# Optimization experiments

Hardware: AMD Instinct MI355X
Metric: run time of the kernel (lower is better)

## Reference

```python
import jax, jax.numpy as jnp
import numpy as np

B_SZ, L_SEQ, H_CH, N_ST = 8, 4096, 256, 64


def setup_inputs() -> dict:
    key = jax.random.key(0)
    ks = jax.random.split(key, 12)
    rn = lambda k, s, sc=1.0: jax.random.normal(k, s, jnp.float32) * sc
    inp = {
        'x': rn(ks[0], (B_SZ, L_SEQ, H_CH)),
        # stable DPLR spectrum: Re(Lambda) < 0, HiPPO-like imaginary ladder
        'Lambda_re': -(jnp.abs(rn(ks[1], (N_ST,))) + 0.1),
        'Lambda_im': jnp.pi * jnp.arange(N_ST, dtype=jnp.float32),
        'P_re': rn(ks[2], (N_ST,), N_ST ** -0.5),
        'P_im': rn(ks[3], (N_ST,), N_ST ** -0.5),
        'Q_re': rn(ks[4], (N_ST,), N_ST ** -0.5),
        'Q_im': rn(ks[5], (N_ST,), N_ST ** -0.5),
        'B_re': rn(ks[6], (N_ST,), N_ST ** -0.5),
        'B_im': rn(ks[7], (N_ST,), N_ST ** -0.5),
        'C_re': rn(ks[8], (H_CH, N_ST), N_ST ** -0.5),
        'C_im': rn(ks[9], (H_CH, N_ST), N_ST ** -0.5),
        'step': jnp.ones((1,), jnp.float32) * 1e-3,
        'D': jnp.zeros((1,), jnp.float32),
        'W_fc': rn(ks[10], (H_CH, H_CH), H_CH ** -0.5),
        'b_fc': jnp.zeros((H_CH,), jnp.float32),
        'ln_g': jnp.ones((H_CH,), jnp.float32),
        'ln_b': jnp.zeros((H_CH,), jnp.float32),
    }
    return inp


def _dplr_kernel(Lambda_re, Lambda_im, P_re, P_im, Q_re, Q_im, B_re, B_im, C_re, C_im, step, L):
    # S4 DPLR generating function evaluated at the L roots of unity (torch_get_K_derta).
    Lam = (Lambda_re + 1j * Lambda_im).astype(jnp.complex64)  # (N,)
    Pc = (P_re + 1j * P_im).astype(jnp.complex64)
    Qc = (Q_re + 1j * Q_im).astype(jnp.complex64)
    Bc = (B_re + 1j * B_im).astype(jnp.complex64)
    Cc = (C_re + 1j * C_im).astype(jnp.complex64)  # (H, N)
    k = jnp.arange(L, dtype=jnp.float32)
    Omega = jnp.exp((-2j * jnp.pi) * (k / L)).astype(jnp.complex64)  # (L,)
    c = 2.0 / (1.0 + Omega)
    g = (2.0 / step[0]) * (1.0 - Omega) / (1.0 + Omega)  # bilinear transform points, (L,)
    inv = 1.0 / (g[:, None] - Lam[None, :])  # Cauchy matrix, (L, N)
    k00 = jnp.einsum('hn,ln->hl', Cc * Bc[None, :], inv)  # (H, L)
    k01 = jnp.einsum('hn,ln->hl', Cc * Pc[None, :], inv)
    k10 = jnp.einsum('n,ln->l', Qc * Bc, inv)  # (L,)
    k11 = jnp.einsum('n,ln->l', Qc * Pc, inv)
    atRoots = c[None, :] * (k00 - k01 * (k10 / (1.0 + k11))[None, :])  # Woodbury correction
    K = jnp.fft.ifft(atRoots, axis=-1).real  # (H, L)
    return K.astype(jnp.float32)


def reference(x, Lambda_re, Lambda_im, P_re, P_im, Q_re, Q_im, B_re, B_im, C_re, C_im, step, D, W_fc, b_fc, ln_g, ln_b):
    Bsz, L, H = x.shape
    step = jnp.maximum(step, 1e-6)
    K = _dplr_kernel(Lambda_re, Lambda_im, P_re, P_im, Q_re, Q_im, B_re, B_im, C_re, C_im, step, L)  # (H, L)
    # causal FFT convolution per channel (torch_convolution with fft=True)
    n = 2 * L
    Kf = jnp.fft.rfft(K, n=n, axis=-1)           # (H, F)
    uf = jnp.fft.rfft(x, n=n, axis=1)            # (B, F, H)
    h1 = jnp.fft.irfft(uf * Kf.T[None], n=n, axis=1)[:, :L, :]
    y1 = jax.nn.gelu(h1 + D * x, approximate=False)  # mult_activation='gelu'
    y2 = jax.nn.gelu(y1 @ W_fc.T + b_fc, approximate=False)  # fc + final_act
    y2 = y2 + x  # skip
    mu = jnp.mean(y2, axis=-1, keepdims=True)
    var = jnp.var(y2, axis=-1, keepdims=True)
    y = (y2 - mu) / jnp.sqrt(var + 1e-5) * ln_g + ln_b  # LayerNorm; dropout p=0
    h_ratio = jnp.max(jnp.abs(y), axis=1) / (jnp.max(jnp.abs(x), axis=1) + 1e-6)  # (B, H)
    return y, h_ratio
```

## Files before the change

### kernel.cpp

```cpp
#include <hip/hip_runtime.h>
#include <math.h>

typedef float2 cf;
typedef __attribute__((ext_vector_type(8))) short bf16x8;
typedef __attribute__((ext_vector_type(4))) float f32x4;

__device__ __forceinline__ cf cmk(float x, float y){ cf r; r.x=x; r.y=y; return r; }
__device__ __forceinline__ cf cml(cf a, cf b){ return cmk(a.x*b.x - a.y*b.y, a.x*b.y + a.y*b.x); }
__device__ __forceinline__ cf cad(cf a, cf b){ return cmk(a.x+b.x, a.y+b.y); }
__device__ __forceinline__ cf csb(cf a, cf b){ return cmk(a.x-b.x, a.y-b.y); }
__device__ __forceinline__ cf cjg(cf a){ return cmk(a.x, -a.y); }
__device__ __forceinline__ cf crcp(cf d){ float r = 1.0f/(d.x*d.x + d.y*d.y); return cmk(d.x*r, -d.y*r); }
__device__ __forceinline__ cf cdv(cf n, cf d){ return cml(n, crcp(d)); }
__device__ __forceinline__ float geluf(float z){ return 0.5f*z*(1.0f + erff(z*0.70710678118654752f)); }

__device__ __forceinline__ cf twid(float f, float sign){
  float h = f * 0.5f;
  float s = __builtin_amdgcn_sinf(h);
  float c0 = __builtin_amdgcn_cosf(h);
  return cmk(c0, sign * s);
}

__device__ __forceinline__ void bfsplit(float v, ushort* h, ushort* l){
  unsigned u = __float_as_uint(v);
  unsigned hr = (u + 0x7FFFu + ((u >> 16) & 1u)) & 0xFFFF0000u;
  *h = (ushort)(hr >> 16);
  float lv = v - __uint_as_float(hr);
  unsigned u2 = __float_as_uint(lv);
  *l = (ushort)((u2 + 0x7FFFu + ((u2 >> 16) & 1u)) >> 16);
}

__device__ __forceinline__ void dif4q(cf& q0, cf& q1, cf& q2, cf& q3, cf w1, float sign){
  cf w2 = cml(w1, w1);
  cf a1 = cad(q0, q2);
  cf c1 = cml(csb(q0, q2), w1);
  cf b1 = cad(q1, q3);
  cf d1 = cml(csb(q1, q3), cmk(-sign*w1.y, sign*w1.x));
  q0 = cad(a1, b1);
  q1 = cml(csb(a1, b1), w2);
  q2 = cad(c1, d1);
  q3 = cml(csb(c1, d1), w2);
}
__device__ __forceinline__ void dit4q(cf& q0, cf& q1, cf& q2, cf& q3, cf w1, float sign){
  cf w2 = cml(w1, w1);
  cf t1 = cml(q1, w2);
  cf a1 = cad(q0, t1), b1 = csb(q0, t1);
  cf t2 = cml(q3, w2);
  cf c1 = cad(q2, t2), d1 = csb(q2, t2);
  cf v1 = cml(c1, w1);
  cf v2 = cml(d1, cmk(-sign*w1.y, sign*w1.x));
  q0 = cad(a1, v1);
  q2 = csb(a1, v1);
  q1 = cad(b1, v2);
  q3 = csb(b1, v2);
}
__device__ __forceinline__ void dif4q0(cf& q0, cf& q1, cf& q2, cf& q3, float sign){
  cf a1 = cad(q0, q2), c1 = csb(q0, q2);
  cf b1 = cad(q1, q3), d0 = csb(q1, q3);
  cf d1 = cmk(-sign*d0.y, sign*d0.x);
  q0 = cad(a1, b1); q1 = csb(a1, b1);
  q2 = cad(c1, d1); q3 = csb(c1, d1);
}
__device__ __forceinline__ void dit4q0(cf& q0, cf& q1, cf& q2, cf& q3, float sign){
  cf a1 = cad(q0, q1), b1 = csb(q0, q1);
  cf c1 = cad(q2, q3), d0 = csb(q2, q3);
  cf v2 = cmk(-sign*d0.y, sign*d0.x);
  q0 = cad(a1, c1); q2 = csb(a1, c1);
  q1 = cad(b1, v2); q3 = csb(b1, v2);
}

__device__ __forceinline__ int brev12(int x){ return (int)(__brev((unsigned)x) >> 20); }
__device__ __forceinline__ int brev13(int x){ return (int)(__brev((unsigned)x) >> 19); }
__device__ __forceinline__ int pidx(int n){ return n + 4*(n>>8); }

template<int N, int SSTART, int TP>
__device__ void fft_dif_r4(cf* __restrict__ a, float sign){
  #pragma unroll
  for (int s = SSTART; s >= 1; s >>= 2){
    __syncthreads();
    #pragma unroll
    for (int g = 0; g < (N >> 2) / TP; g++){
      int w = (int)threadIdx.x + g * TP;
      int j = w & (s - 1);
      int base = ((w & ~(s - 1)) << 2) | j;
      cf A0 = a[base], B0 = a[base + s], C0 = a[base + 2*s], D0 = a[base + 3*s];
      cf w1 = twid((float)j / (float)(2 * s), sign);
      cf w2 = cml(w1, w1);
      cf a1 = cad(A0, C0);
      cf c1 = cml(csb(A0, C0), w1);
      cf b1 = cad(B0, D0);
      cf d1 = cml(csb(B0, D0), cmk(-sign * w1.y, sign * w1.x));
      a[base]         = cad(a1, b1);
      a[base + s]     = cml(csb(a1, b1), w2);
      a[base + 2*s]   = cad(c1, d1);
      a[base + 3*s]   = cml(csb(c1, d1), w2);
    }
  }
  if constexpr ((__builtin_ctz(N) & 1) == 1){
    __syncthreads();
    #pragma unroll
    for (int g = 0; g < (N >> 1) / TP; g++){
      int w = (int)threadIdx.x + g * TP;
      int i = w << 1;
      cf u = a[i], v = a[i + 1];
      a[i] = cad(u, v);
      a[i + 1] = csb(u, v);
    }
  }
  __syncthreads();
}

template<int N, int TP>
__device__ void fft_dit_r4(cf* __restrict__ a, float sign){
  if constexpr ((__builtin_ctz(N) & 1) == 1){
    __syncthreads();
    #pragma unroll
    for (int g = 0; g < (N >> 1) / TP; g++){
      int w = (int)threadIdx.x + g * TP;
      int i = w << 1;
      cf u = a[i], v = a[i + 1];
      a[i] = cad(u, v);
      a[i + 1] = csb(u, v);
    }
  }
  constexpr int S0 = ((__builtin_ctz(N) & 1) == 1) ? 2 : 1;
  #pragma unroll
  for (int s = S0; s <= (N >> 2); s <<= 2){
    __syncthreads();
    #pragma unroll
    for (int g = 0; g < (N >> 2) / TP; g++){
      int w = (int)threadIdx.x + g * TP;
      int j = w & (s - 1);
      int base = ((w & ~(s - 1)) << 2) | j;
      cf A0 = a[base], B0 = a[base + s], C0 = a[base + 2*s], D0 = a[base + 3*s];
      cf w1 = twid((float)j / (float)(2 * s), sign);
      cf w2 = cml(w1, w1);
      cf t1 = cml(B0, w2);
      cf a1 = cad(A0, t1), b1 = csb(A0, t1);
      cf t2 = cml(D0, w2);
      cf c1 = cad(C0, t2), d1 = csb(C0, t2);
      cf v1 = cml(c1, w1);
      cf v2 = cml(d1, cmk(-sign * w1.y, sign * w1.x));
      a[base]         = cad(a1, v1);
      a[base + 2*s]   = csb(a1, v1);
      a[base + s]     = cad(b1, v2);
      a[base + 3*s]   = csb(b1, v2);
    }
  }
  __syncthreads();
}

template<int TP>
__device__ void dif8192_pad_stage(cf* __restrict__ a, float sign){
  __syncthreads();
  #pragma unroll
  for (int g = 0; g < 2048 / TP; g++){
    int w = (int)threadIdx.x + g * TP;
    cf A0 = a[w], B0 = a[w + 2048];
    cf w1 = twid((float)w * (1.0f / 4096.0f), sign);
    cf w2 = cml(w1, w1);
    cf c1 = cml(A0, w1);
    cf d1 = cml(B0, cmk(-sign * w1.y, sign * w1.x));
    a[w]        = cad(A0, B0);
    a[w + 2048] = cml(csb(A0, B0), w2);
    a[w + 4096] = cad(c1, d1);
    a[w + 6144] = cml(csb(c1, d1), w2);
  }
}

__global__ void k_init(unsigned* xmax, unsigned* ymax){
  int i = blockIdx.x * 256 + threadIdx.x;
  if (i < 2048){ xmax[i] = 0u; ymax[i] = 0u; }
}

__global__ __launch_bounds__(256) void k_transpose_x(const float* __restrict__ x,
                                                     float* __restrict__ xT,
                                                     unsigned* __restrict__ xmax){
  __shared__ float tile[64][65];
  __shared__ float red[64][4];
  int b = blockIdx.z;
  int t0 = blockIdx.x * 64;
  int h0 = blockIdx.y * 64;
  int hc = threadIdx.x & 63, tg = threadIdx.x >> 6;
  float pmax = 0.0f;
  #pragma unroll
  for (int q = 0; q < 16; q++){
    int tr = tg + q * 4;
    float v = x[((size_t)(b * 4096 + t0 + tr)) * 256 + h0 + hc];
    tile[tr][hc] = v;
    pmax = fmaxf(pmax, fabsf(v));
  }
  red[hc][tg] = pmax;
  __syncthreads();
  if (threadIdx.x < 64){
    float m = fmaxf(fmaxf(red[threadIdx.x][0], red[threadIdx.x][1]),
                    fmaxf(red[threadIdx.x][2], red[threadIdx.x][3]));
    atomicMax(&xmax[b * 256 + h0 + threadIdx.x], __float_as_uint(m));
  }
  #pragma unroll
  for (int q = 0; q < 16; q++){
    int hr = tg + q * 4;
    xT[((size_t)(b * 256 + h0 + hr)) * 4096 + t0 + hc] = tile[hc][hr];
  }
}

__global__ void k_wsplit(const float* __restrict__ W, ushort* __restrict__ Wh, ushort* __restrict__ Wl){
  int i = blockIdx.x * 256 + threadIdx.x;
  ushort h, l;
  bfsplit(W[i], &h, &l);
  Wh[i] = h; Wl[i] = l;
}

__global__ __launch_bounds__(256) void k_cauchy(
    const float* __restrict__ Lr, const float* __restrict__ Li,
    const float* __restrict__ Pr, const float* __restrict__ Pi,
    const float* __restrict__ Qr, const float* __restrict__ Qi,
    const float* __restrict__ Br, const float* __restrict__ Bi,
    const float* __restrict__ Cr, const float* __restrict__ Ci,
    const float* __restrict__ stepp, cf* __restrict__ A)
{
  __shared__ cf sLam[64], sB[64], sP[64], sQB[64], sQP[64];
  __shared__ cf sInv[64][16];
  __shared__ cf sWood[16], sC[16], sG[16];
  int tid = threadIdx.x;
  int l0 = blockIdx.x * 16;
  float stepv = fmaxf(stepp[0], 1e-6f);
  if (tid < 64){
    cf lam = cmk(Lr[tid], Li[tid]);
    cf b = cmk(Br[tid], Bi[tid]);
    cf p = cmk(Pr[tid], Pi[tid]);
    cf q = cmk(Qr[tid], Qi[tid]);
    sLam[tid] = lam; sB[tid] = b; sP[tid] = p;
    sQB[tid] = cml(q, b);
    sQP[tid] = cml(q, p);
  }
  __syncthreads();
  if (tid < 16){
    int l = l0 + tid;
    float ang = -6.2831855f * ((float)l * (1.0f / 4096.0f));
    cf Om = cmk(cosf(ang), sinf(ang));
    cf den = cmk(1.0f + Om.x, Om.y);
    cf num = cmk(1.0f - Om.x, -Om.y);
    cf rden = crcp(den);
    sC[tid] = cml(cmk(2.0f, 0.0f), rden);
    cf g = cml(num, rden);
    float sc = 2.0f / stepv;
    sG[tid] = cmk(g.x * sc, g.y * sc);
  }
  __syncthreads();
  for (int it = tid; it < 1024; it += 256){
    int n = it >> 4, ll = it & 15;
    sInv[n][ll] = crcp(csb(sG[ll], sLam[n]));
  }
  __syncthreads();
  if (tid < 16){
    cf k10 = cmk(0,0), k11 = cmk(0,0);
    for (int n = 0; n < 64; n++){
      k10 = cad(k10, cml(sQB[n], sInv[n][tid]));
      k11 = cad(k11, cml(sQP[n], sInv[n][tid]));
    }
    sWood[tid] = cdv(k10, cmk(1.0f + k11.x, k11.y));
  }
  __syncthreads();
  int h = tid;
  cf a0[16], a1[16];
  #pragma unroll
  for (int ll = 0; ll < 16; ll++){ a0[ll] = cmk(0,0); a1[ll] = cmk(0,0); }
  for (int n = 0; n < 64; n++){
    cf cc = cmk(Cr[h * 64 + n], Ci[h * 64 + n]);
    cf cb = cml(cc, sB[n]);
    cf cp = cml(cc, sP[n]);
    #pragma unroll
    for (int ll = 0; ll < 16; ll++){
      cf iv = sInv[n][ll];
      a0[ll] = cad(a0[ll], cml(cb, iv));
      a1[ll] = cad(a1[ll], cml(cp, iv));
    }
  }
  cf* dst = A + (size_t)h * 4096 + l0;
  #pragma unroll
  for (int ll = 0; ll < 16; ll++){
    dst[ll] = cml(sC[ll], csb(a0[ll], cml(a1[ll], sWood[ll])));
  }
}

__global__ __launch_bounds__(512) void k_kf(const cf* __restrict__ A, float4* __restrict__ Sab){
  extern __shared__ cf c[];
  int hp = blockIdx.x, tid = threadIdx.x;
  const cf* a1p = A + (size_t)(2 * hp) * 4096;
  const cf* a2p = a1p + 4096;
  for (int l = tid; l < 4096; l += 512){
    int r = brev12(l);
    cf u = a1p[l], w = a2p[l];
    c[r] = cmk(u.x - w.y, u.y + w.x);
  }
  fft_dit_r4<4096, 512>(c, 1.0f);
  float k1[8], k2[8];
  #pragma unroll
  for (int q = 0; q < 8; q++){
    cf w = c[tid + q * 512];
    k1[q] = w.x * (1.0f / 4096.0f);
    k2[q] = w.y * (1.0f / 4096.0f);
  }
  __syncthreads();
  #pragma unroll
  for (int q = 0; q < 8; q++) c[tid + q * 512] = cmk(k1[q], k2[q]);
  dif8192_pad_stage<512>(c, -1.0f);
  fft_dif_r4<8192, 512, 512>(c, -1.0f);
  float4* rec = Sab + (size_t)hp * 4097;
  const float sc = 0.5f * 0.5f * (1.0f / 8192.0f);
  #pragma unroll
  for (int q8 = 0; q8 < 8; q8++){
    int t = tid + 512 * q8;
    int p = t << 1;
    int k = brev13(p);
    int qq = brev13((8192 - k) & 8191);
    cf Zp = c[p], Zq = c[qq];
    float K1x = (Zp.x + Zq.x), K1y = (Zp.y - Zq.y);
    float dx  = (Zp.x - Zq.x), dy  = (Zp.y + Zq.y);
    float K2x = dy, K2y = -dx;
    rec[t] = make_float4((K1x + K2x) * sc, (K1y + K2y) * sc,
                         (K1x - K2x) * sc, (K1y - K2y) * sc);
  }
  if (tid == 0){
    cf Z1 = c[1];
    float K1x = 2.0f * Z1.x, K2x = 2.0f * Z1.y;
    rec[4096] = make_float4((K1x + K2x) * sc, 0.0f, (K1x - K2x) * sc, 0.0f);
  }
}

__global__ __launch_bounds__(256) void k_conv(const float* __restrict__ xT,
                                              const float4* __restrict__ Sab,
                                              const float* __restrict__ Dp,
                                              ushort* __restrict__ y1h,
                                              ushort* __restrict__ y1l){
  __shared__ __align__(16) cf c[8320];
  int blk = blockIdx.x;
  int b = blk >> 7, hp = blk & 127;
  int t = threadIdx.x;
  int lo4 = t & 15, hiT = t >> 4;
  int base0 = lo4 + ((hiT << 1) << 8);
  int base1 = lo4 + ((((hiT << 1) | 1)) << 8);
  int cb0 = pidx((t << 1) << 4);
  int cb1 = pidx(((t << 1) | 1) << 4);
  const float* xs1 = xT + ((size_t)(b * 256 + 2 * hp)) * 4096;
  const float* xs2 = xs1 + 4096;
  cf v[32];
  #pragma unroll
  for (int r = 0; r < 16; r++){
    int n = t + 256 * r;
    v[r] = cmk(xs1[n], xs2[n]);
  }
  #pragma unroll
  for (int r = 0; r < 16; r++)
    v[r + 16] = cml(v[r], twid((float)(t + 256 * r) * (1.0f / 4096.0f), -1.0f));
  #pragma unroll
  for (int r0 = 0; r0 < 4; r0++){
    cf w1 = twid((float)(t + 256 * r0) * (1.0f / 2048.0f), -1.0f);
    dif4q(v[r0], v[r0 + 4], v[r0 + 8], v[r0 + 12], w1, -1.0f);
    dif4q(v[16 + r0], v[16 + r0 + 4], v[16 + r0 + 8], v[16 + r0 + 12], w1, -1.0f);
  }
  {
    cf w1 = twid((float)t * (1.0f / 512.0f), -1.0f);
    #pragma unroll
    for (int g = 0; g < 32; g += 4)
      dif4q(v[g], v[g + 1], v[g + 2], v[g + 3], w1, -1.0f);
  }
  #pragma unroll
  for (int r = 0; r < 32; r++) c[pidx(t + 256 * r)] = v[r];
  __syncthreads();
  #pragma unroll
  for (int u = 0; u < 16; u++){
    v[u]      = c[pidx(base0 + (u << 4))];
    v[16 + u] = c[pidx(base1 + (u << 4))];
  }
  #pragma unroll
  for (int u0 = 0; u0 < 4; u0++){
    cf w1 = twid((float)(lo4 + (u0 << 4)) * (1.0f / 128.0f), -1.0f);
    dif4q(v[u0], v[u0 + 4], v[u0 + 8], v[u0 + 12], w1, -1.0f);
    dif4q(v[16 + u0], v[16 + u0 + 4], v[16 + u0 + 8], v[16 + u0 + 12], w1, -1.0f);
  }
  {
    cf w1 = twid((float)lo4 * (1.0f / 32.0f), -1.0f);
    #pragma unroll
    for (int g = 0; g < 32; g += 4)
      dif4q(v[g], v[g + 1], v[g + 2], v[g + 3], w1, -1.0f);
  }
  #pragma unroll
  for (int u = 0; u < 16; u++){
    c[pidx(base0 + (u << 4))] = v[u];
    c[pidx(base1 + (u << 4))] = v[16 + u];
  }
  __syncthreads();
  #pragma unroll
  for (int k = 0; k < 8; k++){
    float4 q0 = *(const float4*)&c[cb0 + 2 * k];
    float4 q1 = *(const float4*)&c[cb1 + 2 * k];
    v[2 * k]      = cmk(q0.x, q0.y); v[2 * k + 1]      = cmk(q0.z, q0.w);
    v[16 + 2 * k] = cmk(q1.x, q1.y); v[16 + 2 * k + 1] = cmk(q1.z, q1.w);
  }
  #pragma unroll
  for (int u0 = 0; u0 < 4; u0++){
    cf w1 = twid((float)u0 * 0.125f, -1.0f);
    dif4q(v[u0], v[u0 + 4], v[u0 + 8], v[u0 + 12], w1, -1.0f);
    dif4q(v[16 + u0], v[16 + u0 + 4], v[16 + u0 + 8], v[16 + u0 + 12], w1, -1.0f);
  }
  #pragma unroll
  for (int g = 0; g < 32; g += 4) dif4q0(v[g], v[g + 1], v[g + 2], v[g + 3], -1.0f);
  #pragma unroll
  for (int k = 0; k < 8; k++){
    *(float4*)&c[cb0 + 2 * k] = make_float4(v[2*k].x, v[2*k].y, v[2*k+1].x, v[2*k+1].y);
    *(float4*)&c[cb1 + 2 * k] = make_float4(v[16+2*k].x, v[16+2*k].y, v[16+2*k+1].x, v[16+2*k+1].y);
  }
  __syncthreads();
  {
    const float4* rec = Sab + (size_t)hp * 4097;
    #pragma unroll
    for (int q8 = 0; q8 < 16; q8++){
      int th = t + 256 * q8;
      int p = th << 1;
      int k = brev13(p);
      int qq = brev13((8192 - k) & 8191);
      int pi = pidx(p), qi = pidx(qq);
      cf Zp = c[pi], Zq = c[qi];
      float4 r0 = rec[th];
      cf Sap = cmk(r0.x, r0.y), Sbp = cmk(r0.z, r0.w);
      c[pi] = cad(cml(Zp, Sap), cml(cjg(Zq), Sbp));
      c[qi] = cad(cml(Zq, cjg(Sap)), cml(cjg(Zp), cjg(Sbp)));
    }
    if (t == 0){
      float4 e = rec[4096];
      cf Z1 = c[pidx(1)];
      c[pidx(1)] = cad(cml(Z1, cmk(e.x, e.y)), cml(cjg(Z1), cmk(e.z, e.w)));
    }
  }
  __syncthreads();
  #pragma unroll
  for (int k = 0; k < 8; k++){
    float4 q0 = *(const float4*)&c[cb0 + 2 * k];
    float4 q1 = *(const float4*)&c[cb1 + 2 * k];
    v[2 * k]      = cmk(q0.x, q0.y); v[2 * k + 1]      = cmk(q0.z, q0.w);
    v[16 + 2 * k] = cmk(q1.x, q1.y); v[16 + 2 * k + 1] = cmk(q1.z, q1.w);
  }
  #pragma unroll
  for (int g = 0; g < 32; g += 4) dit4q0(v[g], v[g + 1], v[g + 2], v[g + 3], 1.0f);
  #pragma unroll
  for (int u0 = 0; u0 < 4; u0++){
    cf w1 = twid((float)u0 * 0.125f, 1.0f);
    dit4q(v[u0], v[u0 + 4], v[u0 + 8], v[u0 + 12], w1, 1.0f);
    dit4q(v[16 + u0], v[16 + u0 + 4], v[16 + u0 + 8], v[16 + u0 + 12], w1, 1.0f);
  }
  #pragma unroll
  for (int k = 0; k < 8; k++){
    *(float4*)&c[cb0 + 2 * k] = make_float4(v[2*k].x, v[2*k].y, v[2*k+1].x, v[2*k+1].y);
    *(float4*)&c[cb1 + 2 * k] = make_float4(v[16+2*k].x, v[16+2*k].y, v[16+2*k+1].x, v[16+2*k+1].y);
  }
  __syncthreads();
  #pragma unroll
  for (int u = 0; u < 16; u++){
    v[u]      = c[pidx(base0 + (u << 4))];
    v[16 + u] = c[pidx(base1 + (u << 4))];
  }
  {
    cf w1 = twid((float)lo4 * (1.0f / 32.0f), 1.0f);
    #pragma unroll
    for (int g = 0; g < 32; g += 4)
      dit4q(v[g], v[g + 1], v[g + 2], v[g + 3], w1, 1.0f);
  }
  #pragma unroll
  for (int u0 = 0; u0 < 4; u0++){
    cf w1 = twid((float)(lo4 + (u0 << 4)) * (1.0f / 128.0f), 1.0f);
    dit4q(v[u0], v[u0 + 4], v[u0 + 8], v[u0 + 12], w1, 1.0f);
    dit4q(v[16 + u0], v[16 + u0 + 4], v[16 + u0 + 8], v[16 + u0 + 12], w1, 1.0f);
  }
  #pragma unroll
  for (int u = 0; u < 16; u++){
    c[pidx(base0 + (u << 4))] = v[u];
    c[pidx(base1 + (u << 4))] = v[16 + u];
  }
  __syncthreads();
  #pragma unroll
  for (int r = 0; r < 32; r++) v[r] = c[pidx(t + 256 * r)];
  {
    cf w1 = twid((float)t * (1.0f / 512.0f), 1.0f);
    #pragma unroll
    for (int g = 0; g < 32; g += 4)
      dit4q(v[g], v[g + 1], v[g + 2], v[g + 3], w1, 1.0f);
  }
  #pragma unroll
  for (int r0 = 0; r0 < 4; r0++){
    cf w1 = twid((float)(t + 256 * r0) * (1.0f / 2048.0f), 1.0f);
    dit4q(v[r0], v[r0 + 4], v[r0 + 8], v[r0 + 12], w1, 1.0f);
    dit4q(v[16 + r0], v[16 + r0 + 4], v[16 + r0 + 8], v[16 + r0 + 12], w1, 1.0f);
  }
  float Dv = Dp[0];
  size_t base = ((size_t)(b * 256 + 2 * hp)) * 4096;
  #pragma unroll
  for (int r = 0; r < 16; r++){
    int n = t + 256 * r;
    cf w = cad(v[r], cml(v[r + 16], twid((float)n * (1.0f / 4096.0f), 1.0f)));
    float z1 = geluf(fmaf(Dv, xs1[n], w.x));
    float z2 = geluf(fmaf(Dv, xs2[n], w.y));
    ushort h0, l0, h1u, l1;
    bfsplit(z1, &h0, &l0);
    bfsplit(z2, &h1u, &l1);
    y1h[base + n] = h0;         y1l[base + n] = l0;
    y1h[base + 4096 + n] = h1u; y1l[base + 4096 + n] = l1;
  }
}

__global__ __launch_bounds__(256, 3) void k_gemm_ln(
    const ushort* __restrict__ y1h, const ushort* __restrict__ y1l,
    const ushort* __restrict__ Wh, const ushort* __restrict__ Wl,
    const float* __restrict__ bfc, const float* __restrict__ x,
    const float* __restrict__ lng, const float* __restrict__ lnb,
    float* __restrict__ yout, unsigned* __restrict__ ymax)
{
  __shared__ ushort sY[2][64 * 40];
  __shared__ float red1[64][4], red2[64][4];
  int tid = threadIdx.x;
  int l = tid & 63;
  int w = tid >> 6;
  int blk = blockIdx.x;
  int b = blk >> 6;
  int t0 = (blk & 63) * 64;
  int g = l >> 4, cc = l & 15;

  f32x4 acc[4][4];
  #pragma unroll
  for (int m = 0; m < 4; m++)
    #pragma unroll
    for (int n = 0; n < 4; n++)
      acc[m][n] = (f32x4){0.0f, 0.0f, 0.0f, 0.0f};

  int kk = tid >> 3, ts = (tid & 7) * 8;

  #pragma unroll 1
  for (int kc = 0; kc < 256; kc += 32){
    __syncthreads();
    {
      size_t gb = ((size_t)(b * 256 + kc + kk)) * 4096 + t0 + ts;
      float4 vh = *(const float4*)(y1h + gb);
      float4 vl = *(const float4*)(y1l + gb);
      const ushort* ph = (const ushort*)&vh;
      const ushort* pl = (const ushort*)&vl;
      int kblk = kk >> 3, kin = kk & 7;
      #pragma unroll
      for (int e = 0; e < 8; e++){
        int t = ts + e;
        int idx = t * 40 + ((kblk ^ ((t >> 3) & 3)) << 3) + kin;
        sY[0][idx] = ph[e];
        sY[1][idx] = pl[e];
      }
    }
    __syncthreads();
    bf16x8 afh[4], afl[4];
    #pragma unroll
    for (int m = 0; m < 4; m++){
      int t = m * 16 + cc;
      int idx = t * 40 + ((g ^ ((t >> 3) & 3)) << 3);
      afh[m] = *(bf16x8*)&sY[0][idx];
      afl[m] = *(bf16x8*)&sY[1][idx];
    }
    #pragma unroll
    for (int n = 0; n < 4; n++){
      size_t wj = (size_t)(w * 64 + n * 16 + cc) * 256 + kc + g * 8;
      bf16x8 bh = *(const bf16x8*)(Wh + wj);
      bf16x8 bl = *(const bf16x8*)(Wl + wj);
      #pragma unroll
      for (int m = 0; m < 4; m++){
        acc[m][n] = __builtin_amdgcn_mfma_f32_16x16x32_bf16(afh[m], bh, acc[m][n], 0, 0, 0);
        acc[m][n] = __builtin_amdgcn_mfma_f32_16x16x32_bf16(afh[m], bl, acc[m][n], 0, 0, 0);
        acc[m][n] = __builtin_amdgcn_mfma_f32_16x16x32_bf16(afl[m], bh, acc[m][n], 0, 0, 0);
      }
    }
  }

  float bj[4], gj[4], lj[4];
  #pragma unroll
  for (int n = 0; n < 4; n++){
    int j = w * 64 + n * 16 + cc;
    bj[n] = bfc[j]; gj[n] = lng[j]; lj[n] = lnb[j];
  }
  #pragma unroll
  for (int m = 0; m < 4; m++){
    #pragma unroll
    for (int r = 0; r < 4; r++){
      int tl = m * 16 + g * 4 + r;
      size_t rowb = ((size_t)(b * 4096 + t0 + tl)) * 256;
      float ss = 0.0f, sq = 0.0f;
      #pragma unroll
      for (int n = 0; n < 4; n++){
        float z = geluf(acc[m][n][r] + bj[n]) + x[rowb + w * 64 + n * 16 + cc];
        acc[m][n][r] = z;
        ss += z; sq = fmaf(z, z, sq);
      }
      #pragma unroll
      for (int msk = 1; msk < 16; msk <<= 1){
        ss += __shfl_xor(ss, msk);
        sq += __shfl_xor(sq, msk);
      }
      if (cc == 0){ red1[tl][w] = ss; red2[tl][w] = sq; }
    }
  }
  __syncthreads();
  float jm[4] = {0.0f, 0.0f, 0.0f, 0.0f};
  #pragma unroll
  for (int m = 0; m < 4; m++){
    #pragma unroll
    for (int r = 0; r < 4; r++){
      int tl = m * 16 + g * 4 + r;
      float ts1 = red1[tl][0] + red1[tl][1] + red1[tl][2] + red1[tl][3];
      float ts2 = red2[tl][0] + red2[tl][1] + red2[tl][2] + red2[tl][3];
      float mu = ts1 * (1.0f / 256.0f);
      float var = ts2 * (1.0f / 256.0f) - mu * mu;
      float rstd = rsqrtf(var + 1e-5f);
      size_t rowb = ((size_t)(b * 4096 + t0 + tl)) * 256;
      #pragma unroll
      for (int n = 0; n < 4; n++){
        float yv = (acc[m][n][r] - mu) * rstd * gj[n] + lj[n];
        yout[rowb + w * 64 + n * 16 + cc] = yv;
        jm[n] = fmaxf(jm[n], fabsf(yv));
      }
    }
  }
  #pragma unroll
  for (int n = 0; n < 4; n++){
    jm[n] = fmaxf(jm[n], __shfl_xor(jm[n], 16));
    jm[n] = fmaxf(jm[n], __shfl_xor(jm[n], 32));
  }
  if (g == 0){
    #pragma unroll
    for (int n = 0; n < 4; n++)
      atomicMax(&ymax[b * 256 + w * 64 + n * 16 + cc], __float_as_uint(jm[n]));
  }
}

__global__ void k_ratio(const unsigned* __restrict__ ymax, const unsigned* __restrict__ xmax,
                        float* __restrict__ out){
  int i = blockIdx.x * 256 + threadIdx.x;
  if (i < 2048){
    float ym = __uint_as_float(ymax[i]);
    float xm = __uint_as_float(xmax[i]);
    out[8388608 + i] = ym / (xm + 1e-6f);
  }
}

extern "C" void kernel_launch(void* const* d_in, const int* in_sizes, int n_in,
                              void* d_out, int out_size, void* d_ws, size_t ws_size,
                              hipStream_t stream)
{
  const float* x    = (const float*)d_in[0];
  const float* Lr   = (const float*)d_in[1];
  const float* Li   = (const float*)d_in[2];
  const float* Pr   = (const float*)d_in[3];
  const float* Pi   = (const float*)d_in[4];
  const float* Qr   = (const float*)d_in[5];
  const float* Qi   = (const float*)d_in[6];
  const float* Br   = (const float*)d_in[7];
  const float* Bi   = (const float*)d_in[8];
  const float* Cr   = (const float*)d_in[9];
  const float* Ci   = (const float*)d_in[10];
  const float* stp  = (const float*)d_in[11];
  const float* Dp   = (const float*)d_in[12];
  const float* Wfc  = (const float*)d_in[13];
  const float* bfc  = (const float*)d_in[14];
  const float* lng  = (const float*)d_in[15];
  const float* lnb  = (const float*)d_in[16];

  char* ws = (char*)d_ws;
  float*    xT   = (float*)(ws);
  float4*   Sab  = (float4*)(ws + ((size_t)32 << 20));
  cf*       A    = (cf*)(ws + ((size_t)41 << 20));
  ushort*   y1h  = (ushort*)(ws + ((size_t)41 << 20));
  ushort*   y1l  = (ushort*)(ws + ((size_t)57 << 20));
  ushort*   Wh   = (ushort*)(ws + ((size_t)73 << 20));
  ushort*   Wl   = (ushort*)(ws + ((size_t)73 << 20) + (128u << 10));
  unsigned* xmax = (unsigned*)(ws + ((size_t)73 << 20) + (256u << 10));
  unsigned* ymax = xmax + 2048;

  k_init<<<8, 256, 0, stream>>>(xmax, ymax);
  dim3 gt(64, 4, 8);
  k_transpose_x<<<gt, 256, 0, stream>>>(x, xT, xmax);
  k_wsplit<<<256, 256, 0, stream>>>(Wfc, Wh, Wl);
  k_cauchy<<<256, 256, 0, stream>>>(Lr, Li, Pr, Pi, Qr, Qi, Br, Bi, Cr, Ci, stp, A);
  k_kf<<<128, 512, 65536, stream>>>(A, Sab);
  k_conv<<<1024, 256, 0, stream>>>(xT, Sab, Dp, y1h, y1l);
  k_gemm_ln<<<512, 256, 0, stream>>>(y1h, y1l, Wh, Wl, bfc, x, lng, lnb, (float*)d_out, ymax);
  k_ratio<<<8, 256, 0, stream>>>(ymax, xmax, (float*)d_out);
}
```

Measured before the change: 215.3 us.

## Use packed f32 complex ops, fold init into wsplit, widen k_kf blocks

Complex add, sub and mul helpers are rewritten with inline v_pk_add_f32, v_pk_mul_f32 and v_pk_fma_f32 asm, so each complex op uses packed two-lane instructions. The separate k_init launch is removed and the max-buffer zeroing moves into k_wsplit, which now runs before the transpose. k_kf goes from 512 to 1024 threads per block so each of its 128 blocks has more parallelism. Inline asm can block compiler scheduling and fusion, and the larger block may raise register pressure.

```diff
diff --git a/kernel.cpp b/kernel.cpp
--- a/kernel.cpp
+++ b/kernel.cpp
@@ -2,13 +2,33 @@
 #include <math.h>
 
 typedef float2 cf;
+typedef float vf2 __attribute__((ext_vector_type(2)));
 typedef __attribute__((ext_vector_type(8))) short bf16x8;
 typedef __attribute__((ext_vector_type(4))) float f32x4;
 
 __device__ __forceinline__ cf cmk(float x, float y){ cf r; r.x=x; r.y=y; return r; }
-__device__ __forceinline__ cf cml(cf a, cf b){ return cmk(a.x*b.x - a.y*b.y, a.x*b.y + a.y*b.x); }
-__device__ __forceinline__ cf cad(cf a, cf b){ return cmk(a.x+b.x, a.y+b.y); }
-__device__ __forceinline__ cf csb(cf a, cf b){ return cmk(a.x-b.x, a.y-b.y); }
+
+__device__ __forceinline__ cf cad(cf a, cf b){
+  vf2 av, bv, rv;
+  av.x = a.x; av.y = a.y; bv.x = b.x; bv.y = b.y;
+  asm("v_pk_add_f32 %0, %1, %2" : "=v"(rv) : "v"(av), "v"(bv));
+  return cmk(rv.x, rv.y);
+}
+__device__ __forceinline__ cf csb(cf a, cf b){
+  vf2 av, bv, rv;
+  av.x = a.x; av.y = a.y; bv.x = b.x; bv.y = b.y;
+  asm("v_pk_add_f32 %0, %1, %2 neg_lo:[0,1] neg_hi:[0,1]" : "=v"(rv) : "v"(av), "v"(bv));
+  return cmk(rv.x, rv.y);
+}
+__device__ __forceinline__ cf cml(cf a, cf b){
+  vf2 av, bv, rv;
+  av.x = a.x; av.y = a.y; bv.x = b.x; bv.y = b.y;
+  asm("v_pk_mul_f32 %0, %1, %2 op_sel:[0,0] op_sel_hi:[0,1]\n\t"
+      "v_pk_fma_f32 %0, %1, %2, %0 op_sel:[1,1,0] op_sel_hi:[1,0,1] neg_lo:[1,0,0]"
+      : "=&v"(rv) : "v"(av), "v"(bv));
+  return cmk(rv.x, rv.y);
+}
+
 __device__ __forceinline__ cf cjg(cf a){ return cmk(a.x, -a.y); }
 __device__ __forceinline__ cf crcp(cf d){ float r = 1.0f/(d.x*d.x + d.y*d.y); return cmk(d.x*r, -d.y*r); }
 __device__ __forceinline__ cf cdv(cf n, cf d){ return cml(n, crcp(d)); }
@@ -168,11 +188,6 @@
   }
 }
 
-__global__ void k_init(unsigned* xmax, unsigned* ymax){
-  int i = blockIdx.x * 256 + threadIdx.x;
-  if (i < 2048){ xmax[i] = 0u; ymax[i] = 0u; }
-}
-
 __global__ __launch_bounds__(256) void k_transpose_x(const float* __restrict__ x,
                                                      float* __restrict__ xT,
                                                      unsigned* __restrict__ xmax){
@@ -204,8 +219,10 @@
   }
 }
 
-__global__ void k_wsplit(const float* __restrict__ W, ushort* __restrict__ Wh, ushort* __restrict__ Wl){
+__global__ void k_wsplit(const float* __restrict__ W, ushort* __restrict__ Wh, ushort* __restrict__ Wl,
+                         unsigned* __restrict__ xmax, unsigned* __restrict__ ymax){
   int i = blockIdx.x * 256 + threadIdx.x;
+  if (i < 2048){ xmax[i] = 0u; ymax[i] = 0u; }
   ushort h, l;
   bfsplit(W[i], &h, &l);
   Wh[i] = h; Wl[i] = l;
@@ -284,34 +301,34 @@
   }
 }
 
-__global__ __launch_bounds__(512) void k_kf(const cf* __restrict__ A, float4* __restrict__ Sab){
+__global__ __launch_bounds__(1024) void k_kf(const cf* __restrict__ A, float4* __restrict__ Sab){
   extern __shared__ cf c[];
   int hp = blockIdx.x, tid = threadIdx.x;
   const cf* a1p = A + (size_t)(2 * hp) * 4096;
   const cf* a2p = a1p + 4096;
-  for (int l = tid; l < 4096; l += 512){
+  for (int l = tid; l < 4096; l += 1024){
     int r = brev12(l);
     cf u = a1p[l], w = a2p[l];
     c[r] = cmk(u.x - w.y, u.y + w.x);
   }
-  fft_dit_r4<4096, 512>(c, 1.0f);
-  float k1[8], k2[8];
-  #pragma unroll
-  for (int q = 0; q < 8; q++){
-    cf w = c[tid + q * 512];
+  fft_dit_r4<4096, 1024>(c, 1.0f);
+  float k1[4], k2[4];
+  #pragma unroll
+  for (int q = 0; q < 4; q++){
+    cf w = c[tid + q * 1024];
     k1[q] = w.x * (1.0f / 4096.0f);
     k2[q] = w.y * (1.0f / 4096.0f);
   }
   __syncthreads();
   #pragma unroll
-  for (int q = 0; q < 8; q++) c[tid + q * 512] = cmk(k1[q], k2[q]);
-  dif8192_pad_stage<512>(c, -1.0f);
-  fft_dif_r4<8192, 512, 512>(c, -1.0f);
+  for (int q = 0; q < 4; q++) c[tid + q * 1024] = cmk(k1[q], k2[q]);
+  dif8192_pad_stage<1024>(c, -1.0f);
+  fft_dif_r4<8192, 512, 1024>(c, -1.0f);
   float4* rec = Sab + (size_t)hp * 4097;
   const float sc = 0.5f * 0.5f * (1.0f / 8192.0f);
   #pragma unroll
-  for (int q8 = 0; q8 < 8; q8++){
-    int t = tid + 512 * q8;
+  for (int q8 = 0; q8 < 4; q8++){
+    int t = tid + 1024 * q8;
     int p = t << 1;
     int k = brev13(p);
     int qq = brev13((8192 - k) & 8191);
@@ -679,12 +696,11 @@
   unsigned* xmax = (unsigned*)(ws + ((size_t)73 << 20) + (256u << 10));
   unsigned* ymax = xmax + 2048;
 
-  k_init<<<8, 256, 0, stream>>>(xmax, ymax);
+  k_wsplit<<<256, 256, 0, stream>>>(Wfc, Wh, Wl, xmax, ymax);
   dim3 gt(64, 4, 8);
   k_transpose_x<<<gt, 256, 0, stream>>>(x, xT, xmax);
-  k_wsplit<<<256, 256, 0, stream>>>(Wfc, Wh, Wl);
   k_cauchy<<<256, 256, 0, stream>>>(Lr, Li, Pr, Pi, Qr, Qi, Br, Bi, Cr, Ci, stp, A);
-  k_kf<<<128, 512, 65536, stream>>>(A, Sab);
+  k_kf<<<128, 1024, 65536, stream>>>(A, Sab);
   k_conv<<<1024, 256, 0, stream>>>(xT, Sab, Dp, y1h, y1l);
   k_gemm_ln<<<512, 256, 0, stream>>>(y1h, y1l, Wh, Wl, bfc, x, lng, lnb, (float*)d_out, ymax);
   k_ratio<<<8, 256, 0, stream>>>(ymax, xmax, (float*)d_out);
```

After: 183.7 us. 1.17x faster.
